# Performance work log

Hardware: AMD Instinct MI355X
Metric: run time of the kernel (lower is better)

The kernel has to match this reference:

```python
import jax, jax.numpy as jnp
import numpy as np

DIM = 512
NUM_HEADS = 8
HEAD_DIM = DIM // NUM_HEADS
SCALE = HEAD_DIM ** -0.5


def setup_inputs() -> dict:
    key = jax.random.key(0)
    k1, k2, k3, k4 = jax.random.split(key, 4)
    x = jax.random.normal(k1, (2, 4096, DIM), dtype=jnp.float32)
    # Linear weights stored as (in, out) for x @ W; torch Linear(dim, 3*dim, bias=False)
    w_qkv = jax.random.normal(k2, (DIM, 3 * DIM), dtype=jnp.float32) * (DIM ** -0.5)
    w_proj = jax.random.normal(k3, (DIM, DIM), dtype=jnp.float32) * (DIM ** -0.5)
    b_proj = jax.random.normal(k4, (DIM,), dtype=jnp.float32) * 0.02
    return {"x": x, "w_qkv": w_qkv, "w_proj": w_proj, "b_proj": b_proj}


def reference(x, w_qkv, w_proj, b_proj):
    B, N, C = x.shape
    qkv = (x @ w_qkv).reshape(B, N, 3, NUM_HEADS, HEAD_DIM)
    qkv = jnp.transpose(qkv, (2, 0, 3, 1, 4))  # (3, B, H, N, hd)
    q, k, v = qkv[0], qkv[1], qkv[2]
    attn = jnp.einsum("bhnd,bhmd->bhnm", q, k) * SCALE
    attn = jax.nn.softmax(attn, axis=-1)
    out = jnp.einsum("bhnm,bhmd->bhnd", attn, v)
    out = jnp.transpose(out, (0, 2, 1, 3)).reshape(B, N, C)
    return out @ w_proj + b_proj
```

## Files before the change

kernel.cpp:

```cpp
#include <hip/hip_runtime.h>
#include <hip/hip_bf16.h>
#include <stdint.h>
#include <math.h>

#define NC3 1536
#define QSCALE 0.18033688011111907f
#define KSPLIT 2

typedef __attribute__((ext_vector_type(8))) short short8;
typedef __attribute__((ext_vector_type(4))) short short4v;
typedef __attribute__((ext_vector_type(4))) float f32x4;
typedef __attribute__((ext_vector_type(16))) float f32x16;
typedef __attribute__((ext_vector_type(8))) _Float16 f16x8;
typedef __attribute__((ext_vector_type(2))) __fp16 fp16x2;

static __device__ __forceinline__ short f2bf(float f) {
    union { __hip_bfloat16 h; short s; } u;
    u.h = __float2bfloat16(f);
    return u.s;
}
static __device__ __forceinline__ float bf2f(short s) {
    return __uint_as_float(((unsigned)(unsigned short)s) << 16);
}
static __device__ __forceinline__ short f2h(float f) {
    union { __fp16 h; short s; } u;
    u.h = (__fp16)f;
    return u.s;
}
static __device__ __forceinline__ unsigned hpack(float a, float b) {
    union { fp16x2 h; unsigned u; } c;
    c.h = __builtin_amdgcn_cvt_pkrtz(a, b);
    return c.u;
}

#define GLD_LDS(g, l)                                                          \
    __builtin_amdgcn_global_load_lds(                                          \
        (const __attribute__((address_space(1))) void*)(g),                    \
        (__attribute__((address_space(3))) void*)(l), 16, 0, 0)

__global__ __launch_bounds__(256) void prep(const float* __restrict__ x,
                                            short* __restrict__ xbf,
                                            const float* __restrict__ wqkv,
                                            short* __restrict__ wqkvT,
                                            const float* __restrict__ wproj,
                                            short* __restrict__ wprojT) {
    int tx = threadIdx.x, ty = threadIdx.y;
    int tid = ty * 32 + tx;
    if (blockIdx.z == 0) {
        int bid = blockIdx.y * 48 + blockIdx.x;
        for (int i = bid * 256 + tid; i < 1048576; i += 768 * 256) {
            float4 v = ((const float4*)x)[i];
            short4v o = {f2bf(v.x), f2bf(v.y), f2bf(v.z), f2bf(v.w)};
            ((short4v*)xbf)[i] = o;
        }
        return;
    }
    const float* src;
    short* dst;
    int C;
    bool tof16;
    if (blockIdx.z == 1) { src = wqkv; dst = wqkvT; C = 1536; tof16 = false; }
    else                 { if (blockIdx.x >= 16) return; src = wproj; dst = wprojT; C = 512; tof16 = true; }
    __shared__ short t[32][33];
    int c0 = blockIdx.x * 32, r0 = blockIdx.y * 32;
#pragma unroll
    for (int i = 0; i < 4; i++) {
        float v = src[(size_t)(r0 + ty + i * 8) * C + c0 + tx];
        t[ty + i * 8][tx] = tof16 ? f2h(v) : f2bf(v);
    }
    __syncthreads();
#pragma unroll
    for (int i = 0; i < 4; i++)
        dst[(size_t)(c0 + ty + i * 8) * 512 + r0 + tx] = t[tx][ty + i * 8];
}

__global__ __launch_bounds__(256) void gemm_qkv(const short* __restrict__ A,
                                                const short* __restrict__ Bt,
                                                short* __restrict__ Out,
                                                short* __restrict__ VT) {
    __shared__ __attribute__((aligned(16))) short smem[2][128 * 64];
    short* a_sm = &smem[0][0];
    short* b_sm = &smem[1][0];
    const int tid = threadIdx.x;
    const int lane = tid & 63;
    const int wave = tid >> 6;
    const int wr = wave >> 1, wc = wave & 1;
    const int quad = lane >> 4;
    const int l15 = lane & 15;
    const int orig = blockIdx.y * 64 + blockIdx.x;
    const int xcd = orig & 7;
    const int lid = orig >> 3;
    const int m0 = (xcd * 8 + (lid & 7)) * 128;
    const int n0 = (lid >> 3) * 128;
    const int srow = lane >> 3;
    const int schunk = (lane & 7) ^ srow;

    f32x4 zero4 = {0.f, 0.f, 0.f, 0.f};
    f32x4 acc[4][4];
#pragma unroll
    for (int i = 0; i < 4; i++)
#pragma unroll
        for (int j = 0; j < 4; j++) acc[i][j] = zero4;

    for (int k0 = 0; k0 < 512; k0 += 64) {
        __syncthreads();
#pragma unroll
        for (int i = 0; i < 4; i++) {
            int r0 = wave * 32 + i * 8;
            GLD_LDS(A + (size_t)(m0 + r0 + srow) * 512 + k0 + schunk * 8, a_sm + r0 * 64);
            GLD_LDS(Bt + (size_t)(n0 + r0 + srow) * 512 + k0 + schunk * 8, b_sm + r0 * 64);
        }
        __syncthreads();
#pragma unroll
        for (int kk = 0; kk < 2; kk++) {
            short8 af[4], bfr[4];
#pragma unroll
            for (int mi = 0; mi < 4; mi++) {
                int row = wr * 64 + mi * 16 + l15;
                af[mi] = *(const short8*)(a_sm + row * 64 + (((kk * 4 + quad) ^ (row & 7))) * 8);
            }
#pragma unroll
            for (int ni = 0; ni < 4; ni++) {
                int row = wc * 64 + ni * 16 + l15;
                bfr[ni] = *(const short8*)(b_sm + row * 64 + (((kk * 4 + quad) ^ (row & 7))) * 8);
            }
#pragma unroll
            for (int mi = 0; mi < 4; mi++)
#pragma unroll
                for (int ni = 0; ni < 4; ni++)
                    acc[mi][ni] = __builtin_amdgcn_mfma_f32_16x16x32_bf16(
                        af[mi], bfr[ni], acc[mi][ni], 0, 0, 0);
        }
    }

#pragma unroll
    for (int mi = 0; mi < 4; mi++) {
#pragma unroll
        for (int ni = 0; ni < 4; ni++) {
            int gm0 = m0 + wr * 64 + mi * 16 + quad * 4;
            int gn = n0 + wc * 64 + ni * 16 + l15;
            f32x4 v = acc[mi][ni];
#pragma unroll
            for (int r = 0; r < 4; r++) {
                float val = v[r];
                float o = (gn < 512) ? val * QSCALE : val;
                Out[(size_t)(gm0 + r) * NC3 + gn] = f2bf(o);
            }
        }
    }

    if (n0 >= 1024) {
        __syncthreads();
        short* lt = &smem[0][0];
        const int sq = ((quad & 1) << 1) | (quad >> 1);
#pragma unroll
        for (int mi = 0; mi < 4; mi++) {
#pragma unroll
            for (int ni = 0; ni < 4; ni++) {
                int cl = wc * 64 + ni * 16 + l15;
                int tg = wr * 16 + mi * 4 + sq;
                int tg2 = tg ^ ((cl & 7) << 1);
                f32x4 v = acc[mi][ni];
                uint2 pk;
                pk.x = hpack(v[0], v[1]);
                pk.y = hpack(v[2], v[3]);
                *(uint2*)(lt + cl * 128 + tg2 * 4) = pk;
            }
        }
        __syncthreads();
        int cl = tid >> 1, half = tid & 1;
        int cv = n0 - 1024 + cl;
        int h = cv >> 6, d = cv & 63;
        int btok = m0 >> 12;
        int mt = m0 & 4095;
        short* vrow = VT + ((size_t)((btok * 8 + h) * 64 + d)) * 4096 + mt + half * 64;
        int m = (cl & 7) << 1;
#pragma unroll
        for (int j = 0; j < 8; j++) {
            int tg = half * 16 + j * 2;
            short8 v8 = *(const short8*)(lt + cl * 128 + (tg ^ m) * 4);
            *(short8*)(vrow + j * 8) = v8;
        }
    }
}

__global__ __launch_bounds__(256, 4) void attn_kernel(const short* __restrict__ QKV,
                                                      const short* __restrict__ VT,
                                                      short* __restrict__ Op0,
                                                      short* __restrict__ Op1,
                                                      float* __restrict__ lpart) {
    __shared__ __attribute__((aligned(16))) short k_sm[2][64 * 64];
    __shared__ __attribute__((aligned(16))) short v_sm[2][64 * 64];

    const int tid = threadIdx.x;
    const int lane = tid & 63;
    const int wave = tid >> 6;
    const int l31 = lane & 31;
    const int hi = lane >> 5;
    const int orig = (blockIdx.z * 16 + blockIdx.y) * 32 + blockIdx.x;
    const int xcd = orig & 7;
    const int lid = orig >> 3;
    const int qt = lid & 31;
    const int pr = xcd * 4 + (lid >> 5);
    const int bh = pr & 15;
    const int ks = pr >> 4;
    const int b = bh >> 3, h = bh & 7;
    const size_t tokbase = (size_t)b * 4096;
    const int rowbase = qt * 128;
    constexpr int NT = 64 / KSPLIT;
    const int kt0 = ks * NT;
    const int kt1 = kt0 + NT;
    const short* Qg = QKV + h * 64;
    const short* Kg = QKV + 512 + h * 64;
    const short* VTg = VT + (size_t)bh * 64 * 4096;
    const int srow = lane >> 3;
    const int schunk = (lane & 7) ^ srow;

    short* qstage = &k_sm[0][0];
#pragma unroll
    for (int i = 0; i < 4; i++) {
        int r0 = wave * 32 + i * 8;
        GLD_LDS(Qg + (tokbase + rowbase + r0 + srow) * NC3 + schunk * 8, qstage + r0 * 64);
    }
    __syncthreads();
    const int qrow = wave * 32 + l31;
    short8 qf[4];
#pragma unroll
    for (int kk = 0; kk < 4; kk++) {
        int slot = (kk * 2 + hi) ^ (qrow & 7);
        qf[kk] = *(const short8*)(qstage + qrow * 64 + slot * 8);
    }
    __syncthreads();

#pragma unroll
    for (int i = 0; i < 2; i++) {
        int r0 = wave * 16 + i * 8;
        GLD_LDS(Kg + (tokbase + (size_t)kt0 * 64 + r0 + srow) * NC3 + schunk * 8,
                k_sm[0] + r0 * 64);
        GLD_LDS(VTg + (size_t)(r0 + srow) * 4096 + kt0 * 64 + schunk * 8,
                v_sm[0] + r0 * 64);
    }

    f32x16 acc_o0, acc_o1;
#pragma unroll
    for (int i = 0; i < 16; i++) { acc_o0[i] = 0.f; acc_o1[i] = 0.f; }
    float la0 = 0.f, la1 = 0.f;

    for (int kt = kt0; kt < kt1; kt++) {
        __syncthreads();
        const int cur = kt & 1;
        if (kt < kt1 - 1) {
            const int nb = cur ^ 1;
#pragma unroll
            for (int i = 0; i < 2; i++) {
                int r0 = wave * 16 + i * 8;
                GLD_LDS(Kg + (tokbase + (size_t)(kt + 1) * 64 + r0 + srow) * NC3 + schunk * 8,
                        k_sm[nb] + r0 * 64);
                GLD_LDS(VTg + (size_t)(r0 + srow) * 4096 + (kt + 1) * 64 + schunk * 8,
                        v_sm[nb] + r0 * 64);
            }
        }
        __builtin_amdgcn_s_setprio(1);

        f32x16 s0, s1;
#pragma unroll
        for (int i = 0; i < 16; i++) { s0[i] = 0.f; s1[i] = 0.f; }
#pragma unroll
        for (int kk = 0; kk < 4; kk++) {
            int slot = (kk * 2 + hi) ^ (l31 & 7);
            short8 kf0 = *(const short8*)(k_sm[cur] + l31 * 64 + slot * 8);
            s0 = __builtin_amdgcn_mfma_f32_32x32x16_bf16(kf0, qf[kk], s0, 0, 0, 0);
            short8 kf1 = *(const short8*)(k_sm[cur] + (32 + l31) * 64 + slot * 8);
            s1 = __builtin_amdgcn_mfma_f32_32x32x16_bf16(kf1, qf[kk], s1, 0, 0, 0);
        }

        unsigned pk[2][8];
#pragma unroll
        for (int t = 0; t < 16; t += 2) {
            float e0 = __builtin_amdgcn_exp2f(s0[t]);
            float e1 = __builtin_amdgcn_exp2f(s0[t + 1]);
            pk[0][t >> 1] = hpack(e0, e1);
            la0 += e0 + e1;
        }
#pragma unroll
        for (int t = 0; t < 16; t += 2) {
            float e0 = __builtin_amdgcn_exp2f(s1[t]);
            float e1 = __builtin_amdgcn_exp2f(s1[t + 1]);
            pk[1][t >> 1] = hpack(e0, e1);
            la1 += e0 + e1;
        }

#pragma unroll
        for (int g = 0; g < 4; g++) {
            union { unsigned u[4]; f16x8 v; } pf;
#pragma unroll
            for (int t = 0; t < 4; t++) pf.u[t] = pk[g >> 1][4 * (g & 1) + t];
            {
                int slot = (g * 2 + hi) ^ (l31 & 7);
                f16x8 vf0 = *(const f16x8*)(v_sm[cur] + l31 * 64 + slot * 8);
                acc_o0 = __builtin_amdgcn_mfma_f32_32x32x16_f16(vf0, pf.v, acc_o0, 0, 0, 0);
                f16x8 vf1 = *(const f16x8*)(v_sm[cur] + (32 + l31) * 64 + slot * 8);
                acc_o1 = __builtin_amdgcn_mfma_f32_32x32x16_f16(vf1, pf.v, acc_o1, 0, 0, 0);
            }
        }
        __builtin_amdgcn_s_setprio(0);
    }

    __syncthreads();

    float l_acc = la0 + la1;
    l_acc += __shfl_xor(l_acc, 32);
    size_t growq = tokbase + rowbase + qrow;
    if (hi == 0) lpart[(size_t)ks * 65536 + growq * 8 + h] = l_acc;

    short* osm = &k_sm[0][0] + wave * 2048;
#pragma unroll
    for (int i = 0; i < 16; i += 2) {
        int d0 = (i & 3) + 8 * (i >> 2) + 4 * hi;
        unsigned pkd0 = hpack(acc_o0[i], acc_o0[i + 1]);
        int slot0 = (d0 >> 3) ^ (l31 & 7);
        *(unsigned*)(osm + l31 * 64 + slot0 * 8 + (d0 & 7)) = pkd0;
        int d1 = 32 + d0;
        unsigned pkd1 = hpack(acc_o1[i], acc_o1[i + 1]);
        int slot1 = (d1 >> 3) ^ (l31 & 7);
        *(unsigned*)(osm + l31 * 64 + slot1 * 8 + (d1 & 7)) = pkd1;
    }
    short* Od = (ks == 0) ? Op0 : Op1;
#pragma unroll
    for (int j = 0; j < 4; j++) {
        int r = lane >> 1;
        int c = (lane & 1) * 4 + j;
        int slot = c ^ (r & 7);
        short8 ov = *(const short8*)(osm + r * 64 + slot * 8);
        size_t grow = tokbase + rowbase + wave * 32 + r;
        *(short8*)(Od + grow * 512 + h * 64 + c * 8) = ov;
    }
}

__global__ __launch_bounds__(256) void gemm_proj(const short* __restrict__ Op0,
                                                 const short* __restrict__ Op1,
                                                 const float* __restrict__ lpart,
                                                 const short* __restrict__ Bt,
                                                 float* __restrict__ OutF,
                                                 const float* __restrict__ bias) {
    __shared__ __attribute__((aligned(16))) short a0_sm[128 * 64];
    __shared__ __attribute__((aligned(16))) short a1_sm[128 * 64];
    __shared__ __attribute__((aligned(16))) short b_sm[64 * 64];
    __shared__ float linv_sm[128 * 8];
    const int tid = threadIdx.x;
    const int lane = tid & 63;
    const int wave = tid >> 6;
    const int wr = wave >> 1, wc = wave & 1;
    const int quad = lane >> 4;
    const int l15 = lane & 15;
    const int orig = blockIdx.y * 64 + blockIdx.x;
    const int xcd = orig & 7;
    const int lid = orig >> 3;
    const int m0 = (xcd * 8 + (lid & 7)) * 128;
    const int n0 = (lid >> 3) * 64;
    const int srow = lane >> 3;
    const int schunk = (lane & 7) ^ srow;

    {
        int idx = tid * 4;
        int row = idx >> 3;
        int hh = idx & 7;
        float4 va = *(const float4*)(lpart + (size_t)(m0 + row) * 8 + hh);
        float4 vb = *(const float4*)(lpart + 65536 + (size_t)(m0 + row) * 8 + hh);
        linv_sm[idx + 0] = 1.0f / (va.x + vb.x);
        linv_sm[idx + 1] = 1.0f / (va.y + vb.y);
        linv_sm[idx + 2] = 1.0f / (va.z + vb.z);
        linv_sm[idx + 3] = 1.0f / (va.w + vb.w);
    }

    f32x4 zero4 = {0.f, 0.f, 0.f, 0.f};
    f32x4 acc[4][2];
#pragma unroll
    for (int i = 0; i < 4; i++) { acc[i][0] = zero4; acc[i][1] = zero4; }

    for (int k0 = 0; k0 < 512; k0 += 64) {
        __syncthreads();
#pragma unroll
        for (int i = 0; i < 4; i++) {
            int r0 = wave * 32 + i * 8;
            GLD_LDS(Op0 + (size_t)(m0 + r0 + srow) * 512 + k0 + schunk * 8, a0_sm + r0 * 64);
            GLD_LDS(Op1 + (size_t)(m0 + r0 + srow) * 512 + k0 + schunk * 8, a1_sm + r0 * 64);
        }
#pragma unroll
        for (int i = 0; i < 2; i++) {
            int r0 = wave * 16 + i * 8;
            GLD_LDS(Bt + (size_t)(n0 + r0 + srow) * 512 + k0 + schunk * 8, b_sm + r0 * 64);
        }
        __syncthreads();
        const int h = k0 >> 6;
#pragma unroll
        for (int kk = 0; kk < 2; kk++) {
            f16x8 af[4], bfr[2];
#pragma unroll
            for (int mi = 0; mi < 4; mi++) {
                int row = wr * 64 + mi * 16 + l15;
                int slot = (kk * 4 + quad) ^ (row & 7);
                f16x8 a0v = *(const f16x8*)(a0_sm + row * 64 + slot * 8);
                f16x8 a1v = *(const f16x8*)(a1_sm + row * 64 + slot * 8);
                _Float16 lh = (_Float16)linv_sm[row * 8 + h];
                f16x8 lv = {lh, lh, lh, lh, lh, lh, lh, lh};
                af[mi] = (a0v + a1v) * lv;
            }
#pragma unroll
            for (int ni = 0; ni < 2; ni++) {
                int row = wc * 32 + ni * 16 + l15;
                int slot = (kk * 4 + quad) ^ (row & 7);
                bfr[ni] = *(const f16x8*)(b_sm + row * 64 + slot * 8);
            }
#pragma unroll
            for (int mi = 0; mi < 4; mi++)
#pragma unroll
                for (int ni = 0; ni < 2; ni++)
                    acc[mi][ni] = __builtin_amdgcn_mfma_f32_16x16x32_f16(
                        af[mi], bfr[ni], acc[mi][ni], 0, 0, 0);
        }
    }

#pragma unroll
    for (int mi = 0; mi < 4; mi++) {
#pragma unroll
        for (int ni = 0; ni < 2; ni++) {
            int gm0 = m0 + wr * 64 + mi * 16 + quad * 4;
            int gn = n0 + wc * 32 + ni * 16 + l15;
            f32x4 v = acc[mi][ni];
#pragma unroll
            for (int r = 0; r < 4; r++)
                OutF[(size_t)(gm0 + r) * 512 + gn] = v[r] + bias[gn];
        }
    }
}

extern "C" void kernel_launch(void* const* d_in, const int* in_sizes, int n_in,
                              void* d_out, int out_size, void* d_ws, size_t ws_size,
                              hipStream_t stream) {
    (void)in_sizes; (void)n_in; (void)out_size; (void)ws_size;
    const float* x = (const float*)d_in[0];
    const float* wqkv = (const float*)d_in[1];
    const float* wproj = (const float*)d_in[2];
    const float* bproj = (const float*)d_in[3];
    float* out = (float*)d_out;

    short* ws = (short*)d_ws;
    short* xbf = ws;
    short* wqkvT = xbf + (size_t)4194304;
    short* wprojT = wqkvT + (size_t)1536 * 512;
    short* QKV = wprojT + (size_t)512 * 512;
    short* VTb = QKV + (size_t)8192 * 1536;
    short* Op0 = VTb + (size_t)16 * 64 * 4096;
    short* Op1 = xbf;
    float* lpart = (float*)wqkvT;

    prep<<<dim3(48, 16, 3), dim3(32, 8), 0, stream>>>(x, xbf, wqkv, wqkvT, wproj, wprojT);
    gemm_qkv<<<dim3(64, 12), 256, 0, stream>>>(xbf, wqkvT, QKV, VTb);
    attn_kernel<<<dim3(32, 16, KSPLIT), 256, 0, stream>>>(QKV, VTb, Op0, Op1, lpart);
    gemm_proj<<<dim3(64, 8), 256, 0, stream>>>(Op0, Op1, lpart, wprojT, out, bproj);
}
```

Measured before the change: 197.7 us.

## Drop V from QKV buffer, zero-init MFMA accumulators, use fdot2 row sums

The QKV GEMM no longer writes the V columns to the row-major QKV buffer, since V is already stored transposed in VT. The buffer stride shrinks from 1536 to 1024, which cuts global write traffic and gives denser Q/K loads in attention. In the attention loop, the first QK MFMA now takes a zero register vector instead of re-zeroing the accumulators every tile. The softmax row-sum uses fdot2 on the packed fp16 values instead of two float adds. The fdot2 sum accumulates the fp16-rounded probabilities, which matches what the PV MFMA consumes, so precision changes slightly.

Measured after the change: 196.0 us. Within noise of the previous version (-0.9%).

```diff
diff --git a/kernel.cpp b/kernel.cpp
--- a/kernel.cpp
+++ b/kernel.cpp
@@ -4,6 +4,7 @@
 #include <math.h>
 
 #define NC3 1536
+#define NC2 1024
 #define QSCALE 0.18033688011111907f
 #define KSPLIT 2
 
@@ -12,6 +13,7 @@
 typedef __attribute__((ext_vector_type(4))) float f32x4;
 typedef __attribute__((ext_vector_type(16))) float f32x16;
 typedef __attribute__((ext_vector_type(8))) _Float16 f16x8;
+typedef __attribute__((ext_vector_type(2))) _Float16 half2v;
 typedef __attribute__((ext_vector_type(2))) __fp16 fp16x2;
 
 static __device__ __forceinline__ short f2bf(float f) {
@@ -19,9 +21,6 @@
     u.h = __float2bfloat16(f);
     return u.s;
 }
-static __device__ __forceinline__ float bf2f(short s) {
-    return __uint_as_float(((unsigned)(unsigned short)s) << 16);
-}
 static __device__ __forceinline__ short f2h(float f) {
     union { __fp16 h; short s; } u;
     u.h = (__fp16)f;
@@ -31,6 +30,16 @@
     union { fp16x2 h; unsigned u; } c;
     c.h = __builtin_amdgcn_cvt_pkrtz(a, b);
     return c.u;
+}
+static __device__ __forceinline__ float dot2acc(unsigned pu, float c) {
+    union { unsigned u; half2v h; } a;
+    a.u = pu;
+#if __has_builtin(__builtin_amdgcn_fdot2)
+    half2v one2 = {(_Float16)1.0f, (_Float16)1.0f};
+    return __builtin_amdgcn_fdot2(a.h, one2, c, false);
+#else
+    return c + (float)a.h[0] + (float)a.h[1];
+#endif
 }
 
 #define GLD_LDS(g, l)                                                          \
@@ -133,18 +142,20 @@
         }
     }
 
-#pragma unroll
-    for (int mi = 0; mi < 4; mi++) {
-#pragma unroll
-        for (int ni = 0; ni < 4; ni++) {
-            int gm0 = m0 + wr * 64 + mi * 16 + quad * 4;
-            int gn = n0 + wc * 64 + ni * 16 + l15;
-            f32x4 v = acc[mi][ni];
-#pragma unroll
-            for (int r = 0; r < 4; r++) {
-                float val = v[r];
-                float o = (gn < 512) ? val * QSCALE : val;
-                Out[(size_t)(gm0 + r) * NC3 + gn] = f2bf(o);
+    if (n0 < 1024) {
+#pragma unroll
+        for (int mi = 0; mi < 4; mi++) {
+#pragma unroll
+            for (int ni = 0; ni < 4; ni++) {
+                int gm0 = m0 + wr * 64 + mi * 16 + quad * 4;
+                int gn = n0 + wc * 64 + ni * 16 + l15;
+                f32x4 v = acc[mi][ni];
+#pragma unroll
+                for (int r = 0; r < 4; r++) {
+                    float val = v[r];
+                    float o = (gn < 512) ? val * QSCALE : val;
+                    Out[(size_t)(gm0 + r) * NC2 + gn] = f2bf(o);
+                }
             }
         }
     }
@@ -220,7 +231,7 @@
 #pragma unroll
     for (int i = 0; i < 4; i++) {
         int r0 = wave * 32 + i * 8;
-        GLD_LDS(Qg + (tokbase + rowbase + r0 + srow) * NC3 + schunk * 8, qstage + r0 * 64);
+        GLD_LDS(Qg + (tokbase + rowbase + r0 + srow) * NC2 + schunk * 8, qstage + r0 * 64);
     }
     __syncthreads();
     const int qrow = wave * 32 + l31;
@@ -235,12 +246,18 @@
 #pragma unroll
     for (int i = 0; i < 2; i++) {
         int r0 = wave * 16 + i * 8;
-        GLD_LDS(Kg + (tokbase + (size_t)kt0 * 64 + r0 + srow) * NC3 + schunk * 8,
+        GLD_LDS(Kg + (tokbase + (size_t)kt0 * 64 + r0 + srow) * NC2 + schunk * 8,
                 k_sm[0] + r0 * 64);
         GLD_LDS(VTg + (size_t)(r0 + srow) * 4096 + kt0 * 64 + schunk * 8,
                 v_sm[0] + r0 * 64);
     }
 
+    float zf = 0.f;
+    asm volatile("" : "+v"(zf));
+    f32x16 zro;
+#pragma unroll
+    for (int t = 0; t < 16; t++) zro[t] = zf;
+
     f32x16 acc_o0, acc_o1;
 #pragma unroll
     for (int i = 0; i < 16; i++) { acc_o0[i] = 0.f; acc_o1[i] = 0.f; }
@@ -254,7 +271,7 @@
 #pragma unroll
             for (int i = 0; i < 2; i++) {
                 int r0 = wave * 16 + i * 8;
-                GLD_LDS(Kg + (tokbase + (size_t)(kt + 1) * 64 + r0 + srow) * NC3 + schunk * 8,
+                GLD_LDS(Kg + (tokbase + (size_t)(kt + 1) * 64 + r0 + srow) * NC2 + schunk * 8,
                         k_sm[nb] + r0 * 64);
                 GLD_LDS(VTg + (size_t)(r0 + srow) * 4096 + (kt + 1) * 64 + schunk * 8,
                         v_sm[nb] + r0 * 64);
@@ -263,10 +280,15 @@
         __builtin_amdgcn_s_setprio(1);
 
         f32x16 s0, s1;
-#pragma unroll
-        for (int i = 0; i < 16; i++) { s0[i] = 0.f; s1[i] = 0.f; }
-#pragma unroll
-        for (int kk = 0; kk < 4; kk++) {
+        {
+            int slot = hi ^ (l31 & 7);
+            short8 kf0 = *(const short8*)(k_sm[cur] + l31 * 64 + slot * 8);
+            s0 = __builtin_amdgcn_mfma_f32_32x32x16_bf16(kf0, qf[0], zro, 0, 0, 0);
+            short8 kf1 = *(const short8*)(k_sm[cur] + (32 + l31) * 64 + slot * 8);
+            s1 = __builtin_amdgcn_mfma_f32_32x32x16_bf16(kf1, qf[0], zro, 0, 0, 0);
+        }
+#pragma unroll
+        for (int kk = 1; kk < 4; kk++) {
             int slot = (kk * 2 + hi) ^ (l31 & 7);
             short8 kf0 = *(const short8*)(k_sm[cur] + l31 * 64 + slot * 8);
             s0 = __builtin_amdgcn_mfma_f32_32x32x16_bf16(kf0, qf[kk], s0, 0, 0, 0);
@@ -279,15 +301,17 @@
         for (int t = 0; t < 16; t += 2) {
             float e0 = __builtin_amdgcn_exp2f(s0[t]);
             float e1 = __builtin_amdgcn_exp2f(s0[t + 1]);
-            pk[0][t >> 1] = hpack(e0, e1);
-            la0 += e0 + e1;
+            unsigned p = hpack(e0, e1);
+            pk[0][t >> 1] = p;
+            la0 = dot2acc(p, la0);
         }
 #pragma unroll
         for (int t = 0; t < 16; t += 2) {
             float e0 = __builtin_amdgcn_exp2f(s1[t]);
             float e1 = __builtin_amdgcn_exp2f(s1[t + 1]);
-            pk[1][t >> 1] = hpack(e0, e1);
-            la1 += e0 + e1;
+            unsigned p = hpack(e0, e1);
+            pk[1][t >> 1] = p;
+            la1 = dot2acc(p, la1);
         }
 
 #pragma unroll
@@ -450,7 +474,7 @@
     short* wqkvT = xbf + (size_t)4194304;
     short* wprojT = wqkvT + (size_t)1536 * 512;
     short* QKV = wprojT + (size_t)512 * 512;
-    short* VTb = QKV + (size_t)8192 * 1536;
+    short* VTb = QKV + (size_t)8192 * 1024;
     short* Op0 = VTb + (size_t)16 * 64 * 4096;
     short* Op1 = xbf;
     float* lpart = (float*)wqkvT;
```
